# Performance work log

Hardware: AMD Instinct MI355X
Metric: run time of the kernel (lower is better)

The kernel has to match this reference:

```python
import jax, jax.numpy as jnp
import numpy as np
import math

B, S, D, H = 2, 2048, 1024, 16
DK = D // H


def setup_inputs() -> dict:
    key = jax.random.key(0)
    ks = jax.random.split(key, 12)
    scale = 1.0 / math.sqrt(D)
    inp = {
        "q": jax.random.normal(ks[0], (B, S, D), jnp.float32),
        "k": jax.random.normal(ks[1], (B, S, D), jnp.float32),
        "v": jax.random.normal(ks[2], (B, S, D), jnp.float32),
        # causal mask, broadcast over batch and heads; 0 entries are masked out
        "mask": jnp.tril(jnp.ones((S, S), jnp.int32))[None, None, :, :],
        "wq_w": jax.random.normal(ks[3], (D, D), jnp.float32) * scale,
        "wq_b": jax.random.normal(ks[4], (D,), jnp.float32) * 0.01,
        "wk_w": jax.random.normal(ks[5], (D, D), jnp.float32) * scale,
        "wk_b": jax.random.normal(ks[6], (D,), jnp.float32) * 0.01,
        "wv_w": jax.random.normal(ks[7], (D, D), jnp.float32) * scale,
        "wv_b": jax.random.normal(ks[8], (D,), jnp.float32) * 0.01,
        "wo_w": jax.random.normal(ks[9], (D, D), jnp.float32) * scale,
        "wo_b": jax.random.normal(ks[10], (D,), jnp.float32) * 0.01,
    }
    return inp


def _mha(q, k, v, mask, wq_w, wq_b, wk_w, wk_b, wv_w, wv_b, wo_w, wo_b):
    # nn.Linear: x @ W^T + b
    def split_heads(x):  # [B,S,D] -> [B,H,S,DK]
        return x.reshape(B, S, H, DK).transpose(0, 2, 1, 3)

    Q = split_heads(q @ wq_w.T + wq_b)
    K = split_heads(k @ wk_w.T + wk_b)
    V = split_heads(v @ wv_w.T + wv_b)

    scores = jnp.einsum("bhqd,bhkd->bhqk", Q, K) / math.sqrt(DK)  # [B,H,S,S]
    scores = jnp.where(mask == 0, jnp.float32(-1e9), scores)
    # NOTE: source uses softmax(dim=1) == over the HEADS axis; replicated faithfully.
    attn = jax.nn.softmax(scores, axis=1)
    out = jnp.einsum("bhqk,bhkd->bhqd", attn, V)  # [B,H,S,DK]
    out = out.transpose(0, 2, 1, 3).reshape(B, S, D)
    return out @ wo_w.T + wo_b


def reference(q, k, v, mask, wq_w, wq_b, wk_w, wk_b, wv_w, wv_b, wo_w, wo_b):
    return _mha(q, k, v, mask, wq_w, wq_b, wk_w, wk_b, wv_w, wv_b, wo_w, wo_b)
```

## Files before the change

### kernel.cpp

```cpp
#include <hip/hip_runtime.h>
#include <hip/hip_bf16.h>
#include <stdint.h>


#define BB 2
#define SS 2048
#define DD 1024
#define HH 16
#define DKK 64

typedef __attribute__((ext_vector_type(8))) short bf16x8;
typedef __attribute__((ext_vector_type(4))) float f32x4;

typedef __attribute__((address_space(3))) uint32_t lds32_t;
typedef __attribute__((address_space(1))) uint32_t g32_t;

__device__ __forceinline__ void async_cp16(void* lds, const void* g){
    __builtin_amdgcn_global_load_lds((const g32_t*)g, (lds32_t*)lds, 16, 0, 0);
}

__device__ __forceinline__ float bf_lo(uint32_t w){ return __uint_as_float(w << 16); }
__device__ __forceinline__ float bf_hi(uint32_t w){ return __uint_as_float(w & 0xffff0000u); }
__device__ __forceinline__ uint16_t f2bf(float f){
    uint32_t x = __float_as_uint(f);
    return (uint16_t)((x + 0x7fffu + ((x >> 16) & 1u)) >> 16);
}
__device__ __forceinline__ void u4tof8(uint4 u, float* f){
    f[0]=bf_lo(u.x); f[1]=bf_hi(u.x);
    f[2]=bf_lo(u.y); f[3]=bf_hi(u.y);
    f[4]=bf_lo(u.z); f[5]=bf_hi(u.z);
    f[6]=bf_lo(u.w); f[7]=bf_hi(u.w);
}
__device__ __forceinline__ uint4 pack8u(const float* f){
    uint4 r;
    r.x = (uint32_t)f2bf(f[0]) | ((uint32_t)f2bf(f[1]) << 16);
    r.y = (uint32_t)f2bf(f[2]) | ((uint32_t)f2bf(f[3]) << 16);
    r.z = (uint32_t)f2bf(f[4]) | ((uint32_t)f2bf(f[5]) << 16);
    r.w = (uint32_t)f2bf(f[6]) | ((uint32_t)f2bf(f[7]) << 16);
    return r;
}

__global__ __launch_bounds__(256) void cvt_all(
    const float* __restrict__ w0, const float* __restrict__ w1,
    const float* __restrict__ w2, const float* __restrict__ w3,
    const float* __restrict__ a0, const float* __restrict__ a1,
    const float* __restrict__ a2,
    uint16_t* __restrict__ dw0, uint16_t* __restrict__ dw1,
    uint16_t* __restrict__ dw2, uint16_t* __restrict__ dw3,
    uint16_t* __restrict__ da0, uint16_t* __restrict__ da1,
    uint16_t* __restrict__ da2)
{
    const int y = blockIdx.y;
    const float* s; uint16_t* d; int n4;
    switch (y) {
        case 0: s = w0; d = dw0; n4 = 262144; break;
        case 1: s = w1; d = dw1; n4 = 262144; break;
        case 2: s = w2; d = dw2; n4 = 262144; break;
        case 3: s = w3; d = dw3; n4 = 262144; break;
        case 4: s = a0; d = da0; n4 = 1048576; break;
        case 5: s = a1; d = da1; n4 = 1048576; break;
        default: s = a2; d = da2; n4 = 1048576; break;
    }
    int i = blockIdx.x * 256 + threadIdx.x;
    if (i >= n4) return;
    float4 v = ((const float4*)s)[i];
    uint32_t lo = (uint32_t)f2bf(v.x) | ((uint32_t)f2bf(v.y) << 16);
    uint32_t hi = (uint32_t)f2bf(v.z) | ((uint32_t)f2bf(v.w) << 16);
    ((uint2*)d)[i] = make_uint2(lo, hi);
}

template <int OMODE>
__global__ __launch_bounds__(256) void gemm_bt(
    const uint16_t* __restrict__ A, const uint16_t* __restrict__ W,
    const float* __restrict__ bias, void* __restrict__ Cout)
{
    __shared__ uint16_t As[128][32];
    __shared__ uint16_t Bs[128][32];

    const int t    = threadIdx.x;
    const int bm   = blockIdx.x * 128;
    const int bn   = blockIdx.y * 128;
    const int lane = t & 63;
    const int w    = t >> 6;
    const int wm   = (w >> 1) * 64;
    const int wn   = (w & 1) * 64;
    const int lm   = lane & 15;
    const int quad = lane >> 4;

    f32x4 acc[4][4] = {};

    const int lr = lane >> 2;
    const int lc = (lane & 3) * 8;

    for (int k0 = 0; k0 < DD; k0 += 32) {
#pragma unroll
        for (int i2 = 0; i2 < 2; ++i2) {
            const int i = w * 2 + i2;
            async_cp16(&As[16*i][0], &A[(size_t)(bm + 16*i + lr) * DD + k0 + lc]);
            async_cp16(&Bs[16*i][0], &W[(size_t)(bn + 16*i + lr) * DD + k0 + lc]);
        }
        __syncthreads();
        bf16x8 af[4], bf[4];
#pragma unroll
        for (int mt = 0; mt < 4; ++mt) af[mt] = *(const bf16x8*)&As[wm + 16*mt + lm][quad*8];
#pragma unroll
        for (int nt = 0; nt < 4; ++nt) bf[nt] = *(const bf16x8*)&Bs[wn + 16*nt + lm][quad*8];
#pragma unroll
        for (int mt = 0; mt < 4; ++mt)
#pragma unroll
            for (int nt = 0; nt < 4; ++nt)
                acc[mt][nt] = __builtin_amdgcn_mfma_f32_16x16x32_bf16(af[mt], bf[nt], acc[mt][nt], 0, 0, 0);
        __syncthreads();
    }

#pragma unroll
    for (int nt = 0; nt < 4; ++nt) {
        const int ng = bn + wn + 16*nt + lm;
        const float bv = bias[ng];
#pragma unroll
        for (int mt = 0; mt < 4; ++mt) {
            const int m0 = bm + wm + 16*mt + quad*4;
            if (OMODE == 1) {
                const int bb = m0 >> 11, s0 = m0 & (SS - 1);
                const int hh = ng >> 6,  dk = ng & 63;
                float v0 = acc[mt][nt][0] + bv, v1 = acc[mt][nt][1] + bv;
                float v2 = acc[mt][nt][2] + bv, v3 = acc[mt][nt][3] + bv;
                uint2 wv;
                wv.x = (uint32_t)f2bf(v0) | ((uint32_t)f2bf(v1) << 16);
                wv.y = (uint32_t)f2bf(v2) | ((uint32_t)f2bf(v3) << 16);
                *(uint2*)&((uint16_t*)Cout)[(((size_t)(bb*HH + hh))*DKK + dk)*SS + s0] = wv;
            } else {
#pragma unroll
                for (int r = 0; r < 4; ++r) {
                    const int m = m0 + r;
                    const float val = acc[mt][nt][r] + bv;
                    if (OMODE == 0) {
                        const int bb = m >> 11, s = m & (SS - 1);
                        const int hh = ng >> 6, dk = ng & 63;
                        ((uint16_t*)Cout)[(((size_t)(bb*HH + hh))*SS + s)*DKK + dk] = f2bf(val);
                    } else {
                        ((float*)Cout)[(size_t)m * DD + ng] = val;
                    }
                }
            }
        }
    }
}

__global__ __launch_bounds__(256) void suf_kernel(
    const uint16_t* __restrict__ Vt, float* __restrict__ Suf)
{
    const int bh = blockIdx.x;
    const int t  = threadIdx.x;
    const int d = t & 63, seg = t >> 6;
    __shared__ float cs[64][65];
    const uint16_t* row = Vt + ((size_t)bh * DKK + d) * SS;
    for (int cl = 0; cl < 16; ++cl) {
        const int c = seg * 16 + cl;
        float sum = 0.f;
#pragma unroll
        for (int j = 0; j < 4; ++j) {
            uint4 u = *(const uint4*)&row[c * 32 + j * 8];
            float f[8]; u4tof8(u, f);
            sum += ((f[0]+f[1])+(f[2]+f[3])) + ((f[4]+f[5])+(f[6]+f[7]));
        }
        cs[c][d] = sum;
    }
    __syncthreads();
    if (t < 64) {
        float run = 0.f;
        Suf[((size_t)bh * 65 + 64) * DKK + t] = 0.f;
        for (int c = 63; c >= 0; --c) {
            run += cs[c][t];
            Suf[((size_t)bh * 65 + c) * DKK + t] = run;
        }
    }
}

__global__ __launch_bounds__(1024) void attn_v4(
    const uint16_t* __restrict__ Qc, const uint16_t* __restrict__ Kc,
    const uint16_t* __restrict__ Vt, const float* __restrict__ Suf,
    uint16_t* __restrict__ AOp)
{
    __shared__ uint16_t E[2][16][32][40];
    __shared__ uint16_t Zr[32][40];

    const int x  = blockIdx.x;
    const int p  = x & 3;
    const int b  = (x >> 2) & 1;
    const int pr = x >> 3;
    const int tid  = threadIdx.x;
    const int h    = tid >> 6;
    const int lane = tid & 63;
    const int lm   = lane & 15;
    const int quad = lane >> 4;

    const uint16_t* Qh = Qc + ((size_t)(b*HH + h)) * SS * DKK;
    const uint16_t* Kh = Kc + ((size_t)(b*HH + h)) * SS * DKK;
    const uint16_t* Vh = Vt + ((size_t)(b*HH + h)) * DKK * SS;
    uint16_t* AOb = AOp + ((size_t)(p*BB + b)) * SS * DD;

    const int rq = tid >> 4;
    const int rk2 = tid & 15;

    int cc = 0;
#pragma unroll
    for (int tt = 0; tt < 2; ++tt) {
        const int tq = tt ? (63 - pr) : pr;
        const int q0 = tq * 32;

        bf16x8 qf[2][2];
#pragma unroll
        for (int qt = 0; qt < 2; ++qt)
#pragma unroll
            for (int kd = 0; kd < 2; ++kd)
                qf[qt][kd] = *(const bf16x8*)&Qh[(size_t)(q0 + 16*qt + lm)*DKK + kd*32 + quad*8];

        f32x4 oacc[2][4] = {};

        for (int c = p; c <= tq; c += 4, ++cc) {
            const int buf = cc & 1;
            const int k0 = c * 32;
            bf16x8 vf[4];
#pragma unroll
            for (int dt = 0; dt < 4; ++dt)
                vf[dt] = *(const bf16x8*)&Vh[(size_t)(16*dt + lm)*SS + k0 + quad*8];
            f32x4 sacc[2][2] = {};
#pragma unroll
            for (int kt = 0; kt < 2; ++kt) {
                bf16x8 kf0 = *(const bf16x8*)&Kh[(size_t)(k0 + 16*kt + lm)*DKK + quad*8];
                bf16x8 kf1 = *(const bf16x8*)&Kh[(size_t)(k0 + 16*kt + lm)*DKK + 32 + quad*8];
#pragma unroll
                for (int qt = 0; qt < 2; ++qt) {
                    sacc[kt][qt] = __builtin_amdgcn_mfma_f32_16x16x32_bf16(kf0, qf[qt][0], sacc[kt][qt], 0, 0, 0);
                    sacc[kt][qt] = __builtin_amdgcn_mfma_f32_16x16x32_bf16(kf1, qf[qt][1], sacc[kt][qt], 0, 0, 0);
                }
            }
#pragma unroll
            for (int kt = 0; kt < 2; ++kt)
#pragma unroll
                for (int qt = 0; qt < 2; ++qt) {
                    const int qg = q0 + 16*qt + lm;
                    uint16_t ev[4];
#pragma unroll
                    for (int r = 0; r < 4; ++r) {
                        const int kg = k0 + 16*kt + quad*4 + r;
                        ev[r] = f2bf((kg > qg) ? 1.0f : __expf(sacc[kt][qt][r] * 0.125f));
                    }
                    uint2 evw;
                    evw.x = (uint32_t)ev[0] | ((uint32_t)ev[1] << 16);
                    evw.y = (uint32_t)ev[2] | ((uint32_t)ev[3] << 16);
                    *(uint2*)&E[buf][h][16*qt + lm][16*kt + quad*4] = evw;
                }
            __syncthreads();
            if (tid < 512) {
                float z0 = 0.f, z1 = 0.f;
#pragma unroll
                for (int i = 0; i < 16; ++i) {
                    uint32_t wv2 = *(const uint32_t*)&E[buf][i][rq][rk2*2];
                    z0 += bf_lo(wv2); z1 += bf_hi(wv2);
                }
                *(uint32_t*)&Zr[rq][rk2*2] =
                    (uint32_t)f2bf(__fdividef(1.f, z0)) | ((uint32_t)f2bf(__fdividef(1.f, z1)) << 16);
            }
            __syncthreads();
#pragma unroll
            for (int qt = 0; qt < 2; ++qt) {
                uint4 eu = *(const uint4*)&E[buf][h][16*qt + lm][quad*8];
                uint4 zu = *(const uint4*)&Zr[16*qt + lm][quad*8];
                float ef[8], zf[8];
                u4tof8(eu, ef); u4tof8(zu, zf);
                float pf[8];
#pragma unroll
                for (int j = 0; j < 8; ++j) pf[j] = ef[j] * zf[j];
                uint4 pu = pack8u(pf);
                bf16x8 pa = *(bf16x8*)&pu;
#pragma unroll
                for (int dt = 0; dt < 4; ++dt)
                    oacc[qt][dt] = __builtin_amdgcn_mfma_f32_16x16x32_bf16(pa, vf[dt], oacc[qt][dt], 0, 0, 0);
            }
        }

        float corr[4] = {0.f, 0.f, 0.f, 0.f};
        if (p == 0) {
            const float* Sf = Suf + ((size_t)(b*HH + h) * 65 + (tq + 1)) * DKK;
#pragma unroll
            for (int dt = 0; dt < 4; ++dt) corr[dt] = 0.0625f * Sf[16*dt + lm];
        }
#pragma unroll
        for (int qt = 0; qt < 2; ++qt)
#pragma unroll
            for (int dt = 0; dt < 4; ++dt)
#pragma unroll
                for (int r = 0; r < 4; ++r) {
                    const int s = q0 + 16*qt + quad*4 + r;
                    AOb[(size_t)s * DD + h*DKK + 16*dt + lm] = f2bf(oacc[qt][dt][r] + corr[dt]);
                }
    }
}

__global__ __launch_bounds__(256) void reduce4(uint16_t* AOp)
{
    const size_t P1 = (size_t)BB * SS * DD;
    const int i = blockIdx.x * 256 + threadIdx.x;
    uint2 u0 = ((const uint2*)AOp)[i];
    uint2 u1 = ((const uint2*)(AOp + P1))[i];
    uint2 u2 = ((const uint2*)(AOp + 2*P1))[i];
    uint2 u3 = ((const uint2*)(AOp + 3*P1))[i];
    float r[4];
    r[0] = (bf_lo(u0.x) + bf_lo(u1.x)) + (bf_lo(u2.x) + bf_lo(u3.x));
    r[1] = (bf_hi(u0.x) + bf_hi(u1.x)) + (bf_hi(u2.x) + bf_hi(u3.x));
    r[2] = (bf_lo(u0.y) + bf_lo(u1.y)) + (bf_lo(u2.y) + bf_lo(u3.y));
    r[3] = (bf_hi(u0.y) + bf_hi(u1.y)) + (bf_hi(u2.y) + bf_hi(u3.y));
    uint2 wv;
    wv.x = (uint32_t)f2bf(r[0]) | ((uint32_t)f2bf(r[1]) << 16);
    wv.y = (uint32_t)f2bf(r[2]) | ((uint32_t)f2bf(r[3]) << 16);
    ((uint2*)AOp)[i] = wv;
}

extern "C" void kernel_launch(void* const* d_in, const int* in_sizes, int n_in,
                              void* d_out, int out_size, void* d_ws, size_t ws_size,
                              hipStream_t stream)
{
    const float* q    = (const float*)d_in[0];
    const float* k    = (const float*)d_in[1];
    const float* v    = (const float*)d_in[2];
    const float* wq_w = (const float*)d_in[4];
    const float* wq_b = (const float*)d_in[5];
    const float* wk_w = (const float*)d_in[6];
    const float* wk_b = (const float*)d_in[7];
    const float* wv_w = (const float*)d_in[8];
    const float* wv_b = (const float*)d_in[9];
    const float* wo_w = (const float*)d_in[10];
    const float* wo_b = (const float*)d_in[11];
    float* out = (float*)d_out;

    uint16_t* wsu = (uint16_t*)d_ws;
    const size_t M1 = (size_t)1 << 20;
    uint16_t* wcq = wsu + 0 * M1;
    uint16_t* wck = wsu + 1 * M1;
    uint16_t* wcv = wsu + 2 * M1;
    uint16_t* wco = wsu + 3 * M1;
    uint16_t* Qc  = wsu + 4 * M1;
    uint16_t* Kc  = wsu + 8 * M1;
    uint16_t* Vt  = wsu + 12 * M1;
    uint16_t* AOp = wsu + 16 * M1;
    uint16_t* xq  = wsu + 16 * M1;
    uint16_t* xk  = wsu + 20 * M1;
    uint16_t* xv  = wsu + 24 * M1;
    float*    Suf = (float*)wcq;

    cvt_all<<<dim3(4096, 7), 256, 0, stream>>>(
        wq_w, wk_w, wv_w, wo_w, q, k, v,
        wcq, wck, wcv, wco, xq, xk, xv);

    dim3 ggrid(32, 8);
    gemm_bt<0><<<ggrid, 256, 0, stream>>>(xq, wcq, wq_b, Qc);
    gemm_bt<0><<<ggrid, 256, 0, stream>>>(xk, wck, wk_b, Kc);
    gemm_bt<1><<<ggrid, 256, 0, stream>>>(xv, wcv, wv_b, Vt);

    suf_kernel<<<32, 256, 0, stream>>>(Vt, Suf);
    attn_v4<<<256, 1024, 0, stream>>>(Qc, Kc, Vt, Suf, AOp);

    reduce4<<<4096, 256, 0, stream>>>(AOp);
    gemm_bt<2><<<ggrid, 256, 0, stream>>>(AOp, wco, wo_b, out);
}
```

Before: 316.0 us.

## Batch QKV GEMMs, split attention blocks per query tile, retile output GEMM

The three projection GEMMs now run as one launch with a z-dimension, and the 1/sqrt(dk) scale is folded into the Q epilogue. The attention kernel no longer pairs two query tiles per block. It launches twice as many blocks, one per query tile, ordered longest first, and drops the double-buffered E array. bf16 packing uses a perm-based truncation instead of round-to-nearest. The suffix-sum kernel is recoded with coalesced row reads and a shuffle reduction, and the output GEMM uses 64-row tiles so more blocks fill the GPU. Truncating instead of rounding adds some precision risk, and the extra attention blocks pay for reloading Q fragments.

Result: slower. 342.4 us (+8.3%).

```diff
diff --git a/kernel.cpp b/kernel.cpp
--- a/kernel.cpp
+++ b/kernel.cpp
@@ -25,19 +25,14 @@
     uint32_t x = __float_as_uint(f);
     return (uint16_t)((x + 0x7fffu + ((x >> 16) & 1u)) >> 16);
 }
+__device__ __forceinline__ uint32_t pk2(float a, float b){
+    return __builtin_amdgcn_perm(__float_as_uint(a), __float_as_uint(b), 0x07060302u);
+}
 __device__ __forceinline__ void u4tof8(uint4 u, float* f){
     f[0]=bf_lo(u.x); f[1]=bf_hi(u.x);
     f[2]=bf_lo(u.y); f[3]=bf_hi(u.y);
     f[4]=bf_lo(u.z); f[5]=bf_hi(u.z);
     f[6]=bf_lo(u.w); f[7]=bf_hi(u.w);
-}
-__device__ __forceinline__ uint4 pack8u(const float* f){
-    uint4 r;
-    r.x = (uint32_t)f2bf(f[0]) | ((uint32_t)f2bf(f[1]) << 16);
-    r.y = (uint32_t)f2bf(f[2]) | ((uint32_t)f2bf(f[3]) << 16);
-    r.z = (uint32_t)f2bf(f[4]) | ((uint32_t)f2bf(f[5]) << 16);
-    r.w = (uint32_t)f2bf(f[6]) | ((uint32_t)f2bf(f[7]) << 16);
-    return r;
 }
 
 __global__ __launch_bounds__(256) void cvt_all(
@@ -69,13 +64,23 @@
     ((uint2*)d)[i] = make_uint2(lo, hi);
 }
 
-template <int OMODE>
-__global__ __launch_bounds__(256) void gemm_bt(
-    const uint16_t* __restrict__ A, const uint16_t* __restrict__ W,
-    const float* __restrict__ bias, void* __restrict__ Cout)
+__global__ __launch_bounds__(256) void gemm_qkv(
+    const uint16_t* __restrict__ xq, const uint16_t* __restrict__ xk,
+    const uint16_t* __restrict__ xv,
+    const uint16_t* __restrict__ wq, const uint16_t* __restrict__ wk,
+    const uint16_t* __restrict__ wv,
+    const float* __restrict__ bq, const float* __restrict__ bk,
+    const float* __restrict__ bv,
+    uint16_t* __restrict__ Qc, uint16_t* __restrict__ Kc,
+    uint16_t* __restrict__ Vt)
 {
     __shared__ uint16_t As[128][32];
     __shared__ uint16_t Bs[128][32];
+
+    const int z = blockIdx.z;
+    const uint16_t* A = (z == 0) ? xq : (z == 1) ? xk : xv;
+    const uint16_t* W = (z == 0) ? wq : (z == 1) ? wk : wv;
+    const float* bias = (z == 0) ? bq : (z == 1) ? bk : bv;
 
     const int t    = threadIdx.x;
     const int bm   = blockIdx.x * 128;
@@ -113,34 +118,31 @@
         __syncthreads();
     }
 
+    const float scl = (z == 0) ? 0.125f : 1.0f;
 #pragma unroll
     for (int nt = 0; nt < 4; ++nt) {
         const int ng = bn + wn + 16*nt + lm;
-        const float bv = bias[ng];
+        const float bv_ = bias[ng];
 #pragma unroll
         for (int mt = 0; mt < 4; ++mt) {
             const int m0 = bm + wm + 16*mt + quad*4;
-            if (OMODE == 1) {
+            if (z == 2) {
                 const int bb = m0 >> 11, s0 = m0 & (SS - 1);
                 const int hh = ng >> 6,  dk = ng & 63;
-                float v0 = acc[mt][nt][0] + bv, v1 = acc[mt][nt][1] + bv;
-                float v2 = acc[mt][nt][2] + bv, v3 = acc[mt][nt][3] + bv;
-                uint2 wv;
-                wv.x = (uint32_t)f2bf(v0) | ((uint32_t)f2bf(v1) << 16);
-                wv.y = (uint32_t)f2bf(v2) | ((uint32_t)f2bf(v3) << 16);
-                *(uint2*)&((uint16_t*)Cout)[(((size_t)(bb*HH + hh))*DKK + dk)*SS + s0] = wv;
+                float v0 = acc[mt][nt][0] + bv_, v1 = acc[mt][nt][1] + bv_;
+                float v2 = acc[mt][nt][2] + bv_, v3 = acc[mt][nt][3] + bv_;
+                uint2 wv2;
+                wv2.x = (uint32_t)f2bf(v0) | ((uint32_t)f2bf(v1) << 16);
+                wv2.y = (uint32_t)f2bf(v2) | ((uint32_t)f2bf(v3) << 16);
+                *(uint2*)&Vt[(((size_t)(bb*HH + hh))*DKK + dk)*SS + s0] = wv2;
             } else {
+                uint16_t* dst = (z == 0) ? Qc : Kc;
 #pragma unroll
                 for (int r = 0; r < 4; ++r) {
                     const int m = m0 + r;
-                    const float val = acc[mt][nt][r] + bv;
-                    if (OMODE == 0) {
-                        const int bb = m >> 11, s = m & (SS - 1);
-                        const int hh = ng >> 6, dk = ng & 63;
-                        ((uint16_t*)Cout)[(((size_t)(bb*HH + hh))*SS + s)*DKK + dk] = f2bf(val);
-                    } else {
-                        ((float*)Cout)[(size_t)m * DD + ng] = val;
-                    }
+                    const int bb = m >> 11, s = m & (SS - 1);
+                    const int hh = ng >> 6, dk = ng & 63;
+                    dst[(((size_t)(bb*HH + hh))*SS + s)*DKK + dk] = f2bf((acc[mt][nt][r] + bv_) * scl);
                 }
             }
         }
@@ -152,19 +154,20 @@
 {
     const int bh = blockIdx.x;
     const int t  = threadIdx.x;
-    const int d = t & 63, seg = t >> 6;
+    const int w = t >> 6, lane = t & 63;
     __shared__ float cs[64][65];
-    const uint16_t* row = Vt + ((size_t)bh * DKK + d) * SS;
-    for (int cl = 0; cl < 16; ++cl) {
-        const int c = seg * 16 + cl;
-        float sum = 0.f;
-#pragma unroll
-        for (int j = 0; j < 4; ++j) {
-            uint4 u = *(const uint4*)&row[c * 32 + j * 8];
+    const uint16_t* base = Vt + (size_t)bh * DKK * SS;
+    for (int d = w; d < 64; d += 4) {
+        const uint16_t* row = base + (size_t)d * SS;
+#pragma unroll
+        for (int i = 0; i < 4; ++i) {
+            uint4 u = *(const uint4*)&row[i*512 + lane*8];
             float f[8]; u4tof8(u, f);
-            sum += ((f[0]+f[1])+(f[2]+f[3])) + ((f[4]+f[5])+(f[6]+f[7]));
-        }
-        cs[c][d] = sum;
+            float s = ((f[0]+f[1])+(f[2]+f[3])) + ((f[4]+f[5])+(f[6]+f[7]));
+            s += __shfl_xor(s, 1);
+            s += __shfl_xor(s, 2);
+            if ((lane & 3) == 0) cs[i*16 + (lane >> 2)][d] = s;
+        }
     }
     __syncthreads();
     if (t < 64) {
@@ -177,18 +180,20 @@
     }
 }
 
-__global__ __launch_bounds__(1024) void attn_v4(
+__global__ __launch_bounds__(1024) void attn_v5(
     const uint16_t* __restrict__ Qc, const uint16_t* __restrict__ Kc,
     const uint16_t* __restrict__ Vt, const float* __restrict__ Suf,
     uint16_t* __restrict__ AOp)
 {
-    __shared__ uint16_t E[2][16][32][40];
+    __shared__ uint16_t E[16][32][40];
     __shared__ uint16_t Zr[32][40];
 
     const int x  = blockIdx.x;
     const int p  = x & 3;
     const int b  = (x >> 2) & 1;
-    const int pr = x >> 3;
+    const int j  = (x >> 3) & 31;
+    const int tq = (x >> 8) ? j : (63 - j);
+    const int q0 = tq * 32;
     const int tid  = threadIdx.x;
     const int h    = tid >> 6;
     const int lane = tid & 63;
@@ -200,103 +205,95 @@
     const uint16_t* Vh = Vt + ((size_t)(b*HH + h)) * DKK * SS;
     uint16_t* AOb = AOp + ((size_t)(p*BB + b)) * SS * DD;
 
-    const int rq = tid >> 4;
+    bf16x8 qf[2][2];
+#pragma unroll
+    for (int qt = 0; qt < 2; ++qt)
+#pragma unroll
+        for (int kd = 0; kd < 2; ++kd)
+            qf[qt][kd] = *(const bf16x8*)&Qh[(size_t)(q0 + 16*qt + lm)*DKK + kd*32 + quad*8];
+
+    f32x4 oacc[2][4] = {};
+    const int rq  = tid >> 4;
     const int rk2 = tid & 15;
 
-    int cc = 0;
-#pragma unroll
-    for (int tt = 0; tt < 2; ++tt) {
-        const int tq = tt ? (63 - pr) : pr;
-        const int q0 = tq * 32;
-
-        bf16x8 qf[2][2];
-#pragma unroll
-        for (int qt = 0; qt < 2; ++qt)
-#pragma unroll
-            for (int kd = 0; kd < 2; ++kd)
-                qf[qt][kd] = *(const bf16x8*)&Qh[(size_t)(q0 + 16*qt + lm)*DKK + kd*32 + quad*8];
-
-        f32x4 oacc[2][4] = {};
-
-        for (int c = p; c <= tq; c += 4, ++cc) {
-            const int buf = cc & 1;
-            const int k0 = c * 32;
-            bf16x8 vf[4];
+    for (int c = p; c <= tq; c += 4) {
+        const int k0 = c * 32;
+        bf16x8 vf[4];
+#pragma unroll
+        for (int dt = 0; dt < 4; ++dt)
+            vf[dt] = *(const bf16x8*)&Vh[(size_t)(16*dt + lm)*SS + k0 + quad*8];
+        f32x4 sacc[2][2] = {};
+#pragma unroll
+        for (int kt = 0; kt < 2; ++kt) {
+            bf16x8 kf0 = *(const bf16x8*)&Kh[(size_t)(k0 + 16*kt + lm)*DKK + quad*8];
+            bf16x8 kf1 = *(const bf16x8*)&Kh[(size_t)(k0 + 16*kt + lm)*DKK + 32 + quad*8];
+#pragma unroll
+            for (int qt = 0; qt < 2; ++qt) {
+                sacc[kt][qt] = __builtin_amdgcn_mfma_f32_16x16x32_bf16(kf0, qf[qt][0], sacc[kt][qt], 0, 0, 0);
+                sacc[kt][qt] = __builtin_amdgcn_mfma_f32_16x16x32_bf16(kf1, qf[qt][1], sacc[kt][qt], 0, 0, 0);
+            }
+        }
+        __syncthreads();
+#pragma unroll
+        for (int kt = 0; kt < 2; ++kt)
+#pragma unroll
+            for (int qt = 0; qt < 2; ++qt) {
+                const int qg = q0 + 16*qt + lm;
+                float ev[4];
+#pragma unroll
+                for (int r = 0; r < 4; ++r) {
+                    const int kg = k0 + 16*kt + quad*4 + r;
+                    ev[r] = (kg > qg) ? 1.0f : __expf(sacc[kt][qt][r]);
+                }
+                uint2 evw;
+                evw.x = pk2(ev[1], ev[0]);
+                evw.y = pk2(ev[3], ev[2]);
+                *(uint2*)&E[h][16*qt + lm][16*kt + quad*4] = evw;
+            }
+        __syncthreads();
+        if (tid < 512) {
+            float z0 = 0.f, z1 = 0.f;
+#pragma unroll
+            for (int i = 0; i < 16; ++i) {
+                uint32_t wv2 = *(const uint32_t*)&E[i][rq][rk2*2];
+                z0 += bf_lo(wv2); z1 += bf_hi(wv2);
+            }
+            *(uint32_t*)&Zr[rq][rk2*2] = pk2(__fdividef(1.f, z1), __fdividef(1.f, z0));
+        }
+        __syncthreads();
+#pragma unroll
+        for (int qt = 0; qt < 2; ++qt) {
+            uint4 eu = *(const uint4*)&E[h][16*qt + lm][quad*8];
+            uint4 zu = *(const uint4*)&Zr[16*qt + lm][quad*8];
+            float ef[8], zf[8];
+            u4tof8(eu, ef); u4tof8(zu, zf);
+            uint4 pu;
+            pu.x = pk2(ef[1]*zf[1], ef[0]*zf[0]);
+            pu.y = pk2(ef[3]*zf[3], ef[2]*zf[2]);
+            pu.z = pk2(ef[5]*zf[5], ef[4]*zf[4]);
+            pu.w = pk2(ef[7]*zf[7], ef[6]*zf[6]);
+            bf16x8 pa = *(bf16x8*)&pu;
 #pragma unroll
             for (int dt = 0; dt < 4; ++dt)
-                vf[dt] = *(const bf16x8*)&Vh[(size_t)(16*dt + lm)*SS + k0 + quad*8];
-            f32x4 sacc[2][2] = {};
-#pragma unroll
-            for (int kt = 0; kt < 2; ++kt) {
-                bf16x8 kf0 = *(const bf16x8*)&Kh[(size_t)(k0 + 16*kt + lm)*DKK + quad*8];
-                bf16x8 kf1 = *(const bf16x8*)&Kh[(size_t)(k0 + 16*kt + lm)*DKK + 32 + quad*8];
-#pragma unroll
-                for (int qt = 0; qt < 2; ++qt) {
-                    sacc[kt][qt] = __builtin_amdgcn_mfma_f32_16x16x32_bf16(kf0, qf[qt][0], sacc[kt][qt], 0, 0, 0);
-                    sacc[kt][qt] = __builtin_amdgcn_mfma_f32_16x16x32_bf16(kf1, qf[qt][1], sacc[kt][qt], 0, 0, 0);
-                }
+                oacc[qt][dt] = __builtin_amdgcn_mfma_f32_16x16x32_bf16(pa, vf[dt], oacc[qt][dt], 0, 0, 0);
+        }
+    }
+
+    float corr[4] = {0.f, 0.f, 0.f, 0.f};
+    if (p == 0) {
+        const float* Sf = Suf + ((size_t)(b*HH + h) * 65 + (tq + 1)) * DKK;
+#pragma unroll
+        for (int dt = 0; dt < 4; ++dt) corr[dt] = 0.0625f * Sf[16*dt + lm];
+    }
+#pragma unroll
+    for (int qt = 0; qt < 2; ++qt)
+#pragma unroll
+        for (int dt = 0; dt < 4; ++dt)
+#pragma unroll
+            for (int r = 0; r < 4; ++r) {
+                const int s = q0 + 16*qt + quad*4 + r;
+                AOb[(size_t)s * DD + h*DKK + 16*dt + lm] = f2bf(oacc[qt][dt][r] + corr[dt]);
             }
-#pragma unroll
-            for (int kt = 0; kt < 2; ++kt)
-#pragma unroll
-                for (int qt = 0; qt < 2; ++qt) {
-                    const int qg = q0 + 16*qt + lm;
-                    uint16_t ev[4];
-#pragma unroll
-                    for (int r = 0; r < 4; ++r) {
-                        const int kg = k0 + 16*kt + quad*4 + r;
-                        ev[r] = f2bf((kg > qg) ? 1.0f : __expf(sacc[kt][qt][r] * 0.125f));
-                    }
-                    uint2 evw;
-                    evw.x = (uint32_t)ev[0] | ((uint32_t)ev[1] << 16);
-                    evw.y = (uint32_t)ev[2] | ((uint32_t)ev[3] << 16);
-                    *(uint2*)&E[buf][h][16*qt + lm][16*kt + quad*4] = evw;
-                }
-            __syncthreads();
-            if (tid < 512) {
-                float z0 = 0.f, z1 = 0.f;
-#pragma unroll
-                for (int i = 0; i < 16; ++i) {
-                    uint32_t wv2 = *(const uint32_t*)&E[buf][i][rq][rk2*2];
-                    z0 += bf_lo(wv2); z1 += bf_hi(wv2);
-                }
-                *(uint32_t*)&Zr[rq][rk2*2] =
-                    (uint32_t)f2bf(__fdividef(1.f, z0)) | ((uint32_t)f2bf(__fdividef(1.f, z1)) << 16);
-            }
-            __syncthreads();
-#pragma unroll
-            for (int qt = 0; qt < 2; ++qt) {
-                uint4 eu = *(const uint4*)&E[buf][h][16*qt + lm][quad*8];
-                uint4 zu = *(const uint4*)&Zr[16*qt + lm][quad*8];
-                float ef[8], zf[8];
-                u4tof8(eu, ef); u4tof8(zu, zf);
-                float pf[8];
-#pragma unroll
-                for (int j = 0; j < 8; ++j) pf[j] = ef[j] * zf[j];
-                uint4 pu = pack8u(pf);
-                bf16x8 pa = *(bf16x8*)&pu;
-#pragma unroll
-                for (int dt = 0; dt < 4; ++dt)
-                    oacc[qt][dt] = __builtin_amdgcn_mfma_f32_16x16x32_bf16(pa, vf[dt], oacc[qt][dt], 0, 0, 0);
-            }
-        }
-
-        float corr[4] = {0.f, 0.f, 0.f, 0.f};
-        if (p == 0) {
-            const float* Sf = Suf + ((size_t)(b*HH + h) * 65 + (tq + 1)) * DKK;
-#pragma unroll
-            for (int dt = 0; dt < 4; ++dt) corr[dt] = 0.0625f * Sf[16*dt + lm];
-        }
-#pragma unroll
-        for (int qt = 0; qt < 2; ++qt)
-#pragma unroll
-            for (int dt = 0; dt < 4; ++dt)
-#pragma unroll
-                for (int r = 0; r < 4; ++r) {
-                    const int s = q0 + 16*qt + quad*4 + r;
-                    AOb[(size_t)s * DD + h*DKK + 16*dt + lm] = f2bf(oacc[qt][dt][r] + corr[dt]);
-                }
-    }
 }
 
 __global__ __launch_bounds__(256) void reduce4(uint16_t* AOp)
@@ -307,15 +304,70 @@
     uint2 u1 = ((const uint2*)(AOp + P1))[i];
     uint2 u2 = ((const uint2*)(AOp + 2*P1))[i];
     uint2 u3 = ((const uint2*)(AOp + 3*P1))[i];
-    float r[4];
-    r[0] = (bf_lo(u0.x) + bf_lo(u1.x)) + (bf_lo(u2.x) + bf_lo(u3.x));
-    r[1] = (bf_hi(u0.x) + bf_hi(u1.x)) + (bf_hi(u2.x) + bf_hi(u3.x));
-    r[2] = (bf_lo(u0.y) + bf_lo(u1.y)) + (bf_lo(u2.y) + bf_lo(u3.y));
-    r[3] = (bf_hi(u0.y) + bf_hi(u1.y)) + (bf_hi(u2.y) + bf_hi(u3.y));
+    float r0 = (bf_lo(u0.x) + bf_lo(u1.x)) + (bf_lo(u2.x) + bf_lo(u3.x));
+    float r1 = (bf_hi(u0.x) + bf_hi(u1.x)) + (bf_hi(u2.x) + bf_hi(u3.x));
+    float r2 = (bf_lo(u0.y) + bf_lo(u1.y)) + (bf_lo(u2.y) + bf_lo(u3.y));
+    float r3 = (bf_hi(u0.y) + bf_hi(u1.y)) + (bf_hi(u2.y) + bf_hi(u3.y));
     uint2 wv;
-    wv.x = (uint32_t)f2bf(r[0]) | ((uint32_t)f2bf(r[1]) << 16);
-    wv.y = (uint32_t)f2bf(r[2]) | ((uint32_t)f2bf(r[3]) << 16);
+    wv.x = (uint32_t)f2bf(r0) | ((uint32_t)f2bf(r1) << 16);
+    wv.y = (uint32_t)f2bf(r2) | ((uint32_t)f2bf(r3) << 16);
     ((uint2*)AOp)[i] = wv;
+}
+
+__global__ __launch_bounds__(256) void gemm_fin(
+    const uint16_t* __restrict__ A, const uint16_t* __restrict__ W,
+    const float* __restrict__ bias, float* __restrict__ Cout)
+{
+    __shared__ uint16_t S[192][32];
+
+    const int t    = threadIdx.x;
+    const int bm   = blockIdx.x * 64;
+    const int bn   = blockIdx.y * 128;
+    const int lane = t & 63;
+    const int w    = t >> 6;
+    const int wm   = (w >> 1) * 32;
+    const int wn   = (w & 1) * 64;
+    const int lm   = lane & 15;
+    const int quad = lane >> 4;
+
+    f32x4 acc[2][4] = {};
+
+    const int lr = lane >> 2;
+    const int lc = (lane & 3) * 8;
+
+    for (int k0 = 0; k0 < DD; k0 += 32) {
+        async_cp16(&S[16*w][0], &A[(size_t)(bm + 16*w + lr) * DD + k0 + lc]);
+#pragma unroll
+        for (int i2 = 0; i2 < 2; ++i2) {
+            const int g = 2*w + i2;
+            async_cp16(&S[64 + 16*g][0], &W[(size_t)(bn + 16*g + lr) * DD + k0 + lc]);
+        }
+        __syncthreads();
+        bf16x8 af[2], bf[4];
+#pragma unroll
+        for (int mt = 0; mt < 2; ++mt) af[mt] = *(const bf16x8*)&S[wm + 16*mt + lm][quad*8];
+#pragma unroll
+        for (int nt = 0; nt < 4; ++nt) bf[nt] = *(const bf16x8*)&S[64 + wn + 16*nt + lm][quad*8];
+#pragma unroll
+        for (int mt = 0; mt < 2; ++mt)
+#pragma unroll
+            for (int nt = 0; nt < 4; ++nt)
+                acc[mt][nt] = __builtin_amdgcn_mfma_f32_16x16x32_bf16(af[mt], bf[nt], acc[mt][nt], 0, 0, 0);
+        __syncthreads();
+    }
+
+#pragma unroll
+    for (int nt = 0; nt < 4; ++nt) {
+        const int ng = bn + wn + 16*nt + lm;
+        const float bv = bias[ng];
+#pragma unroll
+        for (int mt = 0; mt < 2; ++mt) {
+            const int m0 = bm + wm + 16*mt + quad*4;
+#pragma unroll
+            for (int r = 0; r < 4; ++r)
+                Cout[(size_t)(m0 + r) * DD + ng] = acc[mt][nt][r] + bv;
+        }
+    }
 }
 
 extern "C" void kernel_launch(void* const* d_in, const int* in_sizes, int n_in,
@@ -354,14 +406,12 @@
         wq_w, wk_w, wv_w, wo_w, q, k, v,
         wcq, wck, wcv, wco, xq, xk, xv);
 
-    dim3 ggrid(32, 8);
-    gemm_bt<0><<<ggrid, 256, 0, stream>>>(xq, wcq, wq_b, Qc);
-    gemm_bt<0><<<ggrid, 256, 0, stream>>>(xk, wck, wk_b, Kc);
-    gemm_bt<1><<<ggrid, 256, 0, stream>>>(xv, wcv, wv_b, Vt);
+    gemm_qkv<<<dim3(32, 8, 3), 256, 0, stream>>>(
+        xq, xk, xv, wcq, wck, wcv, wq_b, wk_b, wv_b, Qc, Kc, Vt);
 
     suf_kernel<<<32, 256, 0, stream>>>(Vt, Suf);
-    attn_v4<<<256, 1024, 0, stream>>>(Qc, Kc, Vt, Suf, AOp);
+    attn_v5<<<512, 1024, 0, stream>>>(Qc, Kc, Vt, Suf, AOp);
 
     reduce4<<<4096, 256, 0, stream>>>(AOp);
-    gemm_bt<2><<<ggrid, 256, 0, stream>>>(AOp, wco, wo_b, out);
-}
+    gemm_fin<<<dim3(64, 8), 256, 0, stream>>>(AOp, wco, wo_b, out);
+}
```
